# Optimization experiments

Measured on AMD Instinct MI355X. Metric: run time of the kernel, lower is better.

## Reference

```python
import jax, jax.numpy as jnp
import numpy as np

EMBED_DIM = 1024
N_HEADS = 16
HEAD_DIM = EMBED_DIM // N_HEADS


def setup_inputs() -> dict:
    key = jax.random.key(0)
    k1, k2, k3 = jax.random.split(key, 3)
    B, T, D = 2, 2048, EMBED_DIM
    x = jax.random.normal(k1, (B, T, D), dtype=jnp.float32)
    # torch nn.Linear weights: (out_features, in_features); y = x @ W.T
    scale = 1.0 / np.sqrt(D)
    qkv_w = jax.random.uniform(k2, (3 * D, D), dtype=jnp.float32, minval=-scale, maxval=scale)
    out_w = jax.random.uniform(k3, (D, D), dtype=jnp.float32, minval=-scale, maxval=scale)
    return {"x": x, "qkv_w": qkv_w, "out_w": out_w}


def reference(x, qkv_w, out_w):
    B, T, D = x.shape
    H, hd = N_HEADS, HEAD_DIM
    qkv = jnp.einsum('btd,ed->bte', x, qkv_w)  # (B,T,3D)
    qkv = qkv.reshape(B, T, 3, H, hd)
    q = jnp.transpose(qkv[:, :, 0], (0, 2, 1, 3))  # (B,H,T,hd)
    k = jnp.transpose(qkv[:, :, 1], (0, 2, 1, 3))
    v = jnp.transpose(qkv[:, :, 2], (0, 2, 1, 3))
    scores = jnp.einsum('bhtd,bhsd->bhts', q, k) / np.sqrt(hd).astype(np.float32)
    causal = jnp.tril(jnp.ones((T, T), dtype=bool))  # True = keep
    scores = jnp.where(causal[None, None], scores, -jnp.inf)
    probs = jax.nn.softmax(scores, axis=-1)
    out = jnp.einsum('bhts,bhsd->bhtd', probs, v)
    out = jnp.transpose(out, (0, 2, 1, 3)).reshape(B, T, D)
    return jnp.einsum('btd,ed->bte', out, out_w)
```

## Files before the change

### kernel.cpp

```cpp
#include <hip/hip_runtime.h>
#include <hip/hip_bf16.h>
#include <stdint.h>

typedef __bf16 bf16;
typedef __attribute__((ext_vector_type(8))) __bf16 bf16x8;
typedef __attribute__((ext_vector_type(4))) __bf16 bf16x4;
typedef __attribute__((ext_vector_type(4))) float f32x4;

#define AS1 __attribute__((address_space(1)))
#define AS3 __attribute__((address_space(3)))

__device__ __forceinline__ void async16(const void* g, void* l) {
  __builtin_amdgcn_global_load_lds((AS1 uint32_t*)(g), (AS3 uint32_t*)(l), 16, 0, 0);
}

__device__ __forceinline__ f32x4 mfma_bf16(bf16x8 a, bf16x8 b, f32x4 c) {
  return __builtin_amdgcn_mfma_f32_16x16x32_bf16(a, b, c, 0, 0, 0);
}

__device__ __forceinline__ uint32_t pack2_bf16(float a, float b) {
  union { __hip_bfloat162 h2; uint32_t u; } u;
  u.h2 = __float22bfloat162_rn(float2{a, b});
  return u.u;
}

__global__ __launch_bounds__(256) void cast_all_kernel(
    const float* __restrict__ x, const float* __restrict__ w1,
    const float* __restrict__ w2, bf16* __restrict__ xb,
    bf16* __restrict__ w1b, bf16* __restrict__ w2b) {
  const int bid = blockIdx.x;
  const float* src;
  bf16* dst;
  int base;
  if (bid < 4096) { src = x;  dst = xb;  base = bid; }
  else if (bid < 7168) { src = w1; dst = w1b; base = bid - 4096; }
  else { src = w2; dst = w2b; base = bid - 7168; }
  const int i = (base * 256 + threadIdx.x) * 4;
  const float4 v = *(const float4*)(src + i);
  bf16x4 o;
  o[0] = (bf16)v.x; o[1] = (bf16)v.y; o[2] = (bf16)v.z; o[3] = (bf16)v.w;
  *(bf16x4*)(dst + i) = o;
}

__global__ __launch_bounds__(256) void gemm_qkv_kernel(
    const bf16* __restrict__ A, const bf16* __restrict__ W,
    bf16* __restrict__ QK, bf16* __restrict__ VT) {
  constexpr int K = 1024;
  __shared__ __align__(16) bf16 sm[2 * 128 * 32];
  const int tid = threadIdx.x;
  const int w = tid >> 6, lane = tid & 63;
  const int m0 = blockIdx.x * 128, n0 = blockIdx.y * 128;
  const int wm = (w >> 1) * 64, wn = (w & 1) * 64;
  const int lrow = lane & 15, quad = lane >> 4;
  const int lk = quad * 8;
  f32x4 acc[4][4] = {};

  for (int k0 = 0; k0 < K; k0 += 32) {
#pragma unroll
    for (int i = 0; i < 4; ++i) {
      const int c = tid + 256 * i;
      const bf16* src = (c < 512)
          ? (A + (size_t)(m0 + (c >> 2)) * K + k0 + (c & 3) * 8)
          : (W + (size_t)(n0 + ((c - 512) >> 2)) * K + k0 + (c & 3) * 8);
      async16(src, sm + (w * 64 + i * 256) * 8);
    }
    __syncthreads();
    bf16x8 af[4], bfr[4];
#pragma unroll
    for (int mi = 0; mi < 4; ++mi)
      af[mi] = *(const bf16x8*)&sm[(wm + mi * 16 + lrow) * 32 + lk];
#pragma unroll
    for (int ni = 0; ni < 4; ++ni)
      bfr[ni] = *(const bf16x8*)&sm[128 * 32 + (wn + ni * 16 + lrow) * 32 + lk];
#pragma unroll
    for (int mi = 0; mi < 4; ++mi)
#pragma unroll
      for (int ni = 0; ni < 4; ++ni)
        acc[mi][ni] = mfma_bf16(af[mi], bfr[ni], acc[mi][ni]);
    __syncthreads();
  }

  bf16* s2 = sm;
  const bool isV = (n0 >= 2048);
  const int bb = m0 >> 11;
  const int mt = m0 & 2047;
  if (!isV) {
#pragma unroll
    for (int c = 0; c < 2; ++c) {
      if ((w >> 1) == c) {
#pragma unroll
        for (int mi = 0; mi < 4; ++mi)
#pragma unroll
          for (int ni = 0; ni < 4; ++ni) {
            const int nr = wn + ni * 16 + lrow;
#pragma unroll
            for (int r = 0; r < 4; ++r)
              s2[(mi * 16 + quad * 4 + r) * 128 + nr] = (bf16)acc[mi][ni][r];
          }
      }
      __syncthreads();
#pragma unroll
      for (int p = 0; p < 4; ++p) {
        const int row = p * 16 + (tid >> 4);
        const int colc = (tid & 15) * 8;
        const bf16x8 v = *(const bf16x8*)&s2[row * 128 + colc];
        *(bf16x8*)(QK + (size_t)(m0 + c * 64 + row) * 2048 + n0 + colc) = v;
      }
      __syncthreads();
    }
  } else {
#pragma unroll
    for (int c = 0; c < 2; ++c) {
      if ((w & 1) == c) {
#pragma unroll
        for (int mi = 0; mi < 4; ++mi)
#pragma unroll
          for (int ni = 0; ni < 4; ++ni) {
            const int nl = ni * 16 + lrow;
            bf16x4 pk4;
#pragma unroll
            for (int r = 0; r < 4; ++r) pk4[r] = (bf16)acc[mi][ni][r];
            *(bf16x4*)&s2[nl * 128 + wm + mi * 16 + quad * 4] = pk4;
          }
      }
      __syncthreads();
#pragma unroll
      for (int p = 0; p < 4; ++p) {
        const int row = p * 16 + (tid >> 4);
        const int colc = (tid & 15) * 8;
        const bf16x8 v = *(const bf16x8*)&s2[row * 128 + colc];
        const int vtrow = bb * 1024 + (n0 - 2048) + c * 64 + row;
        *(bf16x8*)(VT + (size_t)vtrow * 2048 + mt + colc) = v;
      }
      __syncthreads();
    }
  }
}

__global__ __launch_bounds__(512) void attn_kernel(
    const bf16* __restrict__ QK, const bf16* __restrict__ VT,
    bf16* __restrict__ AO) {
  __shared__ __align__(16) bf16 sK[2][2][64 * 64];
  __shared__ __align__(16) bf16 sV[2][2][64 * 64];
  const int bid = blockIdx.x;
  const int half = bid >> 8;
  const int i6 = bid & 255;
  const int bh = i6 & 31;
  const int g = half ? (i6 >> 5) : 15 - (i6 >> 5);
  const int b = bh >> 4, h = bh & 15;
  const int tid = threadIdx.x, w = tid >> 6, lane = tid & 63;
  const int qhalf = w >> 1, parity = w & 1;
  const int Q0 = g * 128;
  const int col = lane & 15, quad = lane >> 4;
  const bf16* Qb = QK + (size_t)b * 2048 * 2048 + h * 64;
  const bf16* Kb = Qb + 1024;
  const bf16* Vb = VT + (size_t)bh * 64 * 2048;
  const float NEG_INF = -__builtin_inff();
  constexpr float QSCALE = 0.18033688011112042f;

  union { uint32_t u[4]; bf16x8 v; } ones;
  ones.u[0] = 0x3F803F80u; ones.u[1] = 0x3F803F80u;
  ones.u[2] = 0x3F803F80u; ones.u[3] = 0x3F803F80u;

  int qrow[2];
  bf16x8 qf[2][2];
#pragma unroll
  for (int qtile = 0; qtile < 2; ++qtile) {
    qrow[qtile] = Q0 + qhalf * 32 + qtile * 16 + col;
#pragma unroll
    for (int kk = 0; kk < 2; ++kk) {
      bf16x8 v = *(const bf16x8*)(Qb + (size_t)qrow[qtile] * 2048 + kk * 32 + quad * 8);
#pragma unroll
      for (int e = 0; e < 8; ++e) v[e] = (bf16)((float)v[e] * QSCALE);
      qf[qtile][kk] = v;
    }
  }

  auto stage = [&](int s0, int cur) {
    bf16* dK = &sK[cur][0][0];
    bf16* dV = &sV[cur][0][0];
#pragma unroll
    for (int i = 0; i < 2; ++i) {
      const int L = tid + 512 * i;
      const int buf = L >> 9, Lr = L & 511;
      const int row = Lr >> 3;
      const int ch = (Lr & 7) ^ (row & 7);
      async16(Kb + (size_t)(s0 + buf * 64 + row) * 2048 + ch * 8, dK + L * 8);
    }
#pragma unroll
    for (int i = 0; i < 2; ++i) {
      const int L = tid + 512 * i;
      const int buf = L >> 9, Lr = L & 511;
      const int d = Lr >> 3;
      const int ch = (Lr & 7) ^ (d & 7);
      async16(Vb + (size_t)d * 2048 + s0 + buf * 64 + ch * 8, dV + L * 8);
    }
  };

  int srow[4];
#pragma unroll
  for (int m = 0; m < 4; ++m)
    srow[m] = 32 * (m & 1) + (col >> 2) * 8 + 4 * (m >> 1) + (col & 3);

  f32x4 accO[4][2] = {};
  f32x4 accL[2] = {};

  auto body = [&](int kv0, bool masked, int cur) {
    const bf16* kbuf = &sK[cur][parity][0];
    const bf16* vbuf = &sV[cur][parity][0];

    f32x4 st[2][4] = {};
#pragma unroll
    for (int kk = 0; kk < 2; ++kk) {
      bf16x8 kf[4];
#pragma unroll
      for (int m = 0; m < 4; ++m)
        kf[m] = *(const bf16x8*)&kbuf[srow[m] * 64 + (((kk * 4 + quad) ^ (srow[m] & 7)) * 8)];
      __builtin_amdgcn_s_setprio(1);
#pragma unroll
      for (int m = 0; m < 4; ++m)
#pragma unroll
        for (int qtile = 0; qtile < 2; ++qtile)
          st[qtile][m] = mfma_bf16(kf[m], qf[qtile][kk], st[qtile][m]);
      __builtin_amdgcn_s_setprio(0);
    }

    if (masked) {
#pragma unroll
      for (int qtile = 0; qtile < 2; ++qtile)
#pragma unroll
        for (int m = 0; m < 4; ++m) {
          const int kvb = kv0 + 32 * (m & 1) + quad * 8 + 4 * (m >> 1);
#pragma unroll
          for (int r = 0; r < 4; ++r)
            st[qtile][m][r] = (kvb + r <= qrow[qtile]) ? st[qtile][m][r] : NEG_INF;
        }
    }

    uint32_t pk[2][4][2];
#pragma unroll
    for (int qtile = 0; qtile < 2; ++qtile)
#pragma unroll
      for (int m = 0; m < 4; ++m) {
        const float p0 = __builtin_amdgcn_exp2f(st[qtile][m][0]);
        const float p1 = __builtin_amdgcn_exp2f(st[qtile][m][1]);
        const float p2 = __builtin_amdgcn_exp2f(st[qtile][m][2]);
        const float p3 = __builtin_amdgcn_exp2f(st[qtile][m][3]);
        pk[qtile][m][0] = pack2_bf16(p0, p1);
        pk[qtile][m][1] = pack2_bf16(p2, p3);
      }

#pragma unroll
    for (int kk = 0; kk < 2; ++kk) {
      bf16x8 vf[4];
#pragma unroll
      for (int d = 0; d < 4; ++d) {
        const int row = d * 16 + col;
        vf[d] = *(const bf16x8*)&vbuf[row * 64 + (((kk * 4 + quad) ^ (row & 7)) * 8)];
      }
      __builtin_amdgcn_s_setprio(1);
#pragma unroll
      for (int qtile = 0; qtile < 2; ++qtile) {
        union { uint32_t u[4]; bf16x8 v; } f;
        f.u[0] = pk[qtile][kk][0];
        f.u[1] = pk[qtile][kk][1];
        f.u[2] = pk[qtile][2 + kk][0];
        f.u[3] = pk[qtile][2 + kk][1];
        accL[qtile] = mfma_bf16(ones.v, f.v, accL[qtile]);
#pragma unroll
        for (int d = 0; d < 4; ++d)
          accO[d][qtile] = mfma_bf16(vf[d], f.v, accO[d][qtile]);
      }
      __builtin_amdgcn_s_setprio(0);
    }
  };

  const int npairs = g + 1;
  const int qmax = Q0 + qhalf * 32 + 31;
  stage(0, 0);
  asm volatile("s_waitcnt vmcnt(0)" ::: "memory");
  __builtin_amdgcn_s_barrier();
  int cur = 0;
  for (int j = 0; j < npairs; ++j) {
    if (j + 1 < npairs) stage((j + 1) * 128, cur ^ 1);
    const int kv0 = j * 128 + parity * 64;
    if (kv0 <= qmax)
      body(kv0, kv0 + 64 > Q0 + qhalf * 32, cur);
    asm volatile("s_waitcnt vmcnt(0)" ::: "memory");
    __builtin_amdgcn_s_barrier();
    cur ^= 1;
  }

  float* scrO = (float*)sK;
  float* scrL = (float*)sV;
  if (parity == 1) {
    const int base = qhalf * 2048;
#pragma unroll
    for (int d = 0; d < 4; ++d)
#pragma unroll
      for (int qtile = 0; qtile < 2; ++qtile)
#pragma unroll
        for (int r = 0; r < 4; ++r)
          scrO[base + ((d * 2 + qtile) * 4 + r) * 64 + lane] = accO[d][qtile][r];
#pragma unroll
    for (int qtile = 0; qtile < 2; ++qtile)
      scrL[qhalf * 128 + qtile * 64 + lane] = accL[qtile][0];
  }
  __syncthreads();
  if (parity == 0) {
    const int base = qhalf * 2048;
#pragma unroll
    for (int d = 0; d < 4; ++d)
#pragma unroll
      for (int qtile = 0; qtile < 2; ++qtile)
#pragma unroll
        for (int r = 0; r < 4; ++r)
          accO[d][qtile][r] += scrO[base + ((d * 2 + qtile) * 4 + r) * 64 + lane];
    bf16* Ob = AO + (size_t)b * 2048 * 1024 + h * 64;
#pragma unroll
    for (int qtile = 0; qtile < 2; ++qtile) {
      const float inv = 1.0f / (accL[qtile][0] + scrL[qhalf * 128 + qtile * 64 + lane]);
#pragma unroll
      for (int d = 0; d < 4; ++d) {
        bf16x4 o;
#pragma unroll
        for (int r = 0; r < 4; ++r) o[r] = (bf16)(accO[d][qtile][r] * inv);
        *(bf16x4*)(Ob + (size_t)qrow[qtile] * 1024 + d * 16 + quad * 4) = o;
      }
    }
  }
}

__global__ __launch_bounds__(256) void gemm_out_kernel(
    const bf16* __restrict__ A, const bf16* __restrict__ W,
    float* __restrict__ C) {
  constexpr int K = 1024;
  __shared__ __align__(16) bf16 sm[2 * 128 * 32];
  const int tid = threadIdx.x;
  const int w = tid >> 6, lane = tid & 63;
  const int m0 = blockIdx.x * 128, n0 = blockIdx.y * 128;
  const int wm = (w >> 1) * 64, wn = (w & 1) * 64;
  const int lrow = lane & 15, lk = (lane >> 4) * 8;
  f32x4 acc[4][4] = {};

  for (int k0 = 0; k0 < K; k0 += 32) {
#pragma unroll
    for (int i = 0; i < 4; ++i) {
      const int c = tid + 256 * i;
      const bf16* src = (c < 512)
          ? (A + (size_t)(m0 + (c >> 2)) * K + k0 + (c & 3) * 8)
          : (W + (size_t)(n0 + ((c - 512) >> 2)) * K + k0 + (c & 3) * 8);
      async16(src, sm + (w * 64 + i * 256) * 8);
    }
    __syncthreads();
    bf16x8 af[4], bfr[4];
#pragma unroll
    for (int mi = 0; mi < 4; ++mi)
      af[mi] = *(const bf16x8*)&sm[(wm + mi * 16 + lrow) * 32 + lk];
#pragma unroll
    for (int ni = 0; ni < 4; ++ni)
      bfr[ni] = *(const bf16x8*)&sm[128 * 32 + (wn + ni * 16 + lrow) * 32 + lk];
#pragma unroll
    for (int mi = 0; mi < 4; ++mi)
#pragma unroll
      for (int ni = 0; ni < 4; ++ni)
        acc[mi][ni] = mfma_bf16(af[mi], bfr[ni], acc[mi][ni]);
    __syncthreads();
  }

#pragma unroll
  for (int mi = 0; mi < 4; ++mi)
#pragma unroll
    for (int ni = 0; ni < 4; ++ni) {
      const int n = n0 + wn + ni * 16 + lrow;
#pragma unroll
      for (int r = 0; r < 4; ++r) {
        const int m = m0 + wm + mi * 16 + (lane >> 4) * 4 + r;
        C[(size_t)m * 1024 + n] = acc[mi][ni][r];
      }
    }
}

extern "C" void kernel_launch(void* const* d_in, const int* in_sizes, int n_in,
                              void* d_out, int out_size, void* d_ws, size_t ws_size,
                              hipStream_t stream) {
  const float* x     = (const float*)d_in[0];
  const float* qkv_w = (const float*)d_in[1];
  const float* out_w = (const float*)d_in[2];
  float* out = (float*)d_out;

  char* ws = (char*)d_ws;
  bf16* xb    = (bf16*)(ws);
  bf16* aob   = (bf16*)(ws);
  bf16* wqkvb = (bf16*)(ws + 8u * 1024 * 1024);
  bf16* wob   = (bf16*)(ws + 14u * 1024 * 1024);
  bf16* qkb   = (bf16*)(ws + 16u * 1024 * 1024);
  bf16* vtb   = (bf16*)(ws + 32u * 1024 * 1024);

  cast_all_kernel<<<8192, 256, 0, stream>>>(x, qkv_w, out_w, xb, wqkvb, wob);
  gemm_qkv_kernel<<<dim3(32, 24), 256, 0, stream>>>(xb, wqkvb, qkb, vtb);
  attn_kernel<<<dim3(512), 512, 0, stream>>>(qkb, vtb, aob);
  gemm_out_kernel<<<dim3(32, 8), 256, 0, stream>>>(aob, wob, out);
}
```

Baseline: 173.3 us.

## Rewrite QKV GEMM with 256x256 tiles, double-buffered async loads and swizzled LDS

The QKV projection GEMM moves from 128x128 tiles with 256 threads and a single-stage load per k-step to 256x256 tiles with 512 threads, BK=64 and double-buffered LDS. Loads for the next k-tile are issued in quarters between MFMA phases using explicit waitcnt/barriers and setprio, so global traffic overlaps compute. XOR swizzling is applied to LDS reads and to the epilogue staging to cut bank conflicts. The trade-off is fewer blocks (192) on a 256-CU part and 128KB of LDS per block, which may hurt occupancy and load balance.

Result: slower. 182.9 us (+5.5%).

```diff
diff --git a/kernel.cpp b/kernel.cpp
--- a/kernel.cpp
+++ b/kernel.cpp
@@ -42,97 +42,134 @@
   *(bf16x4*)(dst + i) = o;
 }
 
-__global__ __launch_bounds__(256) void gemm_qkv_kernel(
+__global__ __launch_bounds__(512, 2) void gemm_qkv_kernel(
     const bf16* __restrict__ A, const bf16* __restrict__ W,
     bf16* __restrict__ QK, bf16* __restrict__ VT) {
   constexpr int K = 1024;
-  __shared__ __align__(16) bf16 sm[2 * 128 * 32];
+  constexpr int NT = 16;
+  __shared__ __align__(16) bf16 smem[4][16384];
   const int tid = threadIdx.x;
-  const int w = tid >> 6, lane = tid & 63;
-  const int m0 = blockIdx.x * 128, n0 = blockIdx.y * 128;
-  const int wm = (w >> 1) * 64, wn = (w & 1) * 64;
+  const int wid = tid >> 6, lane = tid & 63;
+  const int wm = wid >> 2, wn = wid & 3;
   const int lrow = lane & 15, quad = lane >> 4;
-  const int lk = quad * 8;
-  f32x4 acc[4][4] = {};
-
-  for (int k0 = 0; k0 < K; k0 += 32) {
-#pragma unroll
-    for (int i = 0; i < 4; ++i) {
-      const int c = tid + 256 * i;
-      const bf16* src = (c < 512)
-          ? (A + (size_t)(m0 + (c >> 2)) * K + k0 + (c & 3) * 8)
-          : (W + (size_t)(n0 + ((c - 512) >> 2)) * K + k0 + (c & 3) * 8);
-      async16(src, sm + (w * 64 + i * 256) * 8);
-    }
+  const int m0 = blockIdx.x * 256, n0 = blockIdx.y * 256;
+  f32x4 acc[8][4] = {};
+
+  auto stageHT = [&](const bf16* Base, int rowbase, bf16* dst, int h, int kt) {
+#pragma unroll
+    for (int i = 0; i < 2; ++i) {
+      const int L = i * 512 + tid;
+      const int r = L >> 3, cp = L & 7;
+      const int c = cp ^ (((r >> 2) & 1) << 1);
+      async16(Base + (size_t)(rowbase + h * 128 + r) * K + kt * 64 + c * 8,
+              dst + h * 8192 + (i * 512 + wid * 64) * 8);
+    }
+  };
+
+  stageHT(A, m0, smem[0], 0, 0);
+  stageHT(W, n0, smem[2], 0, 0);
+  stageHT(W, n0, smem[2], 1, 0);
+  stageHT(A, m0, smem[0], 1, 0);
+  asm volatile("s_waitcnt vmcnt(0)" ::: "memory");
+  __builtin_amdgcn_s_barrier();
+
+  bf16x8 af[2][4];
+  for (int t = 0; t < NT; ++t) {
+    const bf16* a = smem[t & 1];
+    const bf16* bq = smem[2 + (t & 1)];
+    bf16* na = smem[(t + 1) & 1];
+    bf16* nb = smem[2 + ((t + 1) & 1)];
+    const bool more = (t + 1 < NT);
+#pragma unroll
+    for (int p = 0; p < 4; ++p) {
+      const int mh = p >> 1, nh = p & 1;
+      if ((p & 1) == 0) {
+#pragma unroll
+        for (int kk = 0; kk < 2; ++kk)
+#pragma unroll
+          for (int mi = 0; mi < 4; ++mi) {
+            const int row = wm * 128 + (mh * 4 + mi) * 16 + lrow;
+            const int c = (kk * 4 + quad) ^ (((lrow >> 2) & 1) << 1);
+            af[kk][mi] = *(const bf16x8*)&a[row * 64 + c * 8];
+          }
+      }
+      bf16x8 bf[2][2];
+#pragma unroll
+      for (int kk = 0; kk < 2; ++kk)
+#pragma unroll
+        for (int ni = 0; ni < 2; ++ni) {
+          const int row = wn * 64 + (nh * 2 + ni) * 16 + lrow;
+          const int c = (kk * 4 + quad) ^ (((lrow >> 2) & 1) << 1);
+          bf[kk][ni] = *(const bf16x8*)&bq[row * 64 + c * 8];
+        }
+      if (more) {
+        if (p == 0)      stageHT(A, m0, na, 0, t + 1);
+        else if (p == 1) stageHT(W, n0, nb, 0, t + 1);
+        else if (p == 2) stageHT(W, n0, nb, 1, t + 1);
+        else             stageHT(A, m0, na, 1, t + 1);
+      }
+      asm volatile("s_waitcnt vmcnt(4)" ::: "memory");
+      __builtin_amdgcn_s_barrier();
+      asm volatile("s_waitcnt lgkmcnt(0)" ::: "memory");
+      __builtin_amdgcn_sched_barrier(0);
+      __builtin_amdgcn_s_setprio(1);
+#pragma unroll
+      for (int kk = 0; kk < 2; ++kk)
+#pragma unroll
+        for (int mi = 0; mi < 4; ++mi)
+#pragma unroll
+          for (int ni = 0; ni < 2; ++ni)
+            acc[mh * 4 + mi][nh * 2 + ni] =
+                mfma_bf16(af[kk][mi], bf[kk][ni], acc[mh * 4 + mi][nh * 2 + ni]);
+      __builtin_amdgcn_s_setprio(0);
+      __builtin_amdgcn_s_barrier();
+    }
+  }
+
+  __syncthreads();
+  bf16* cs = &smem[0][0];
+  const bool isV = (n0 >= 2048);
+  if (!isV) {
+#pragma unroll
+    for (int mi = 0; mi < 8; ++mi)
+#pragma unroll
+      for (int ni = 0; ni < 4; ++ni) {
+        const int n = wn * 64 + ni * 16 + lrow;
+#pragma unroll
+        for (int r = 0; r < 4; ++r) {
+          const int m = wm * 128 + mi * 16 + quad * 4 + r;
+          cs[m * 256 + (n ^ ((m & 7) << 3))] = (bf16)acc[mi][ni][r];
+        }
+      }
     __syncthreads();
-    bf16x8 af[4], bfr[4];
-#pragma unroll
-    for (int mi = 0; mi < 4; ++mi)
-      af[mi] = *(const bf16x8*)&sm[(wm + mi * 16 + lrow) * 32 + lk];
-#pragma unroll
-    for (int ni = 0; ni < 4; ++ni)
-      bfr[ni] = *(const bf16x8*)&sm[128 * 32 + (wn + ni * 16 + lrow) * 32 + lk];
-#pragma unroll
-    for (int mi = 0; mi < 4; ++mi)
-#pragma unroll
-      for (int ni = 0; ni < 4; ++ni)
-        acc[mi][ni] = mfma_bf16(af[mi], bfr[ni], acc[mi][ni]);
+#pragma unroll
+    for (int it = 0; it < 16; ++it) {
+      const int L = it * 512 + tid;
+      const int m = L >> 5, nc = L & 31;
+      const bf16x8 v = *(const bf16x8*)&cs[m * 256 + (nc ^ (m & 7)) * 8];
+      *(bf16x8*)(QK + (size_t)(m0 + m) * 2048 + n0 + nc * 8) = v;
+    }
+  } else {
+#pragma unroll
+    for (int mi = 0; mi < 8; ++mi)
+#pragma unroll
+      for (int ni = 0; ni < 4; ++ni) {
+        const int n = wn * 64 + ni * 16 + lrow;
+        const int mb = wm * 128 + mi * 16 + quad * 4;
+        bf16x4 pk;
+#pragma unroll
+        for (int r = 0; r < 4; ++r) pk[r] = (bf16)acc[mi][ni][r];
+        *(bf16x4*)&cs[n * 256 + (mb ^ ((n & 7) << 3))] = pk;
+      }
     __syncthreads();
-  }
-
-  bf16* s2 = sm;
-  const bool isV = (n0 >= 2048);
-  const int bb = m0 >> 11;
-  const int mt = m0 & 2047;
-  if (!isV) {
-#pragma unroll
-    for (int c = 0; c < 2; ++c) {
-      if ((w >> 1) == c) {
-#pragma unroll
-        for (int mi = 0; mi < 4; ++mi)
-#pragma unroll
-          for (int ni = 0; ni < 4; ++ni) {
-            const int nr = wn + ni * 16 + lrow;
-#pragma unroll
-            for (int r = 0; r < 4; ++r)
-              s2[(mi * 16 + quad * 4 + r) * 128 + nr] = (bf16)acc[mi][ni][r];
-          }
-      }
-      __syncthreads();
-#pragma unroll
-      for (int p = 0; p < 4; ++p) {
-        const int row = p * 16 + (tid >> 4);
-        const int colc = (tid & 15) * 8;
-        const bf16x8 v = *(const bf16x8*)&s2[row * 128 + colc];
-        *(bf16x8*)(QK + (size_t)(m0 + c * 64 + row) * 2048 + n0 + colc) = v;
-      }
-      __syncthreads();
-    }
-  } else {
-#pragma unroll
-    for (int c = 0; c < 2; ++c) {
-      if ((w & 1) == c) {
-#pragma unroll
-        for (int mi = 0; mi < 4; ++mi)
-#pragma unroll
-          for (int ni = 0; ni < 4; ++ni) {
-            const int nl = ni * 16 + lrow;
-            bf16x4 pk4;
-#pragma unroll
-            for (int r = 0; r < 4; ++r) pk4[r] = (bf16)acc[mi][ni][r];
-            *(bf16x4*)&s2[nl * 128 + wm + mi * 16 + quad * 4] = pk4;
-          }
-      }
-      __syncthreads();
-#pragma unroll
-      for (int p = 0; p < 4; ++p) {
-        const int row = p * 16 + (tid >> 4);
-        const int colc = (tid & 15) * 8;
-        const bf16x8 v = *(const bf16x8*)&s2[row * 128 + colc];
-        const int vtrow = bb * 1024 + (n0 - 2048) + c * 64 + row;
-        *(bf16x8*)(VT + (size_t)vtrow * 2048 + mt + colc) = v;
-      }
-      __syncthreads();
+    const int bb = m0 >> 11, mt = m0 & 2047;
+#pragma unroll
+    for (int it = 0; it < 16; ++it) {
+      const int L = it * 512 + tid;
+      const int n = L >> 5, mc = L & 31;
+      const bf16x8 v = *(const bf16x8*)&cs[n * 256 + (mc ^ (n & 7)) * 8];
+      const int vtrow = bb * 1024 + (n0 - 2048) + n;
+      *(bf16x8*)(VT + (size_t)vtrow * 2048 + mt + mc * 8) = v;
     }
   }
 }
@@ -398,7 +435,7 @@
   bf16* vtb   = (bf16*)(ws + 32u * 1024 * 1024);
 
   cast_all_kernel<<<8192, 256, 0, stream>>>(x, qkv_w, out_w, xb, wqkvb, wob);
-  gemm_qkv_kernel<<<dim3(32, 24), 256, 0, stream>>>(xb, wqkvb, qkb, vtb);
+  gemm_qkv_kernel<<<dim3(16, 12), 512, 0, stream>>>(xb, wqkvb, qkb, vtb);
   attn_kernel<<<dim3(512), 512, 0, stream>>>(qkb, vtb, aob);
   gemm_out_kernel<<<dim3(32, 8), 256, 0, stream>>>(aob, wob, out);
 }
```
